# Optimization experiments

Measured on AMD Instinct MI355X. Metric: run time of the kernel, lower is better.

Reference implementation:

```python
import jax, jax.numpy as jnp
import numpy as np

ENC_DIM = 1024
NUM_HEADS = 16
HEAD_DIM = ENC_DIM // NUM_HEADS
D_FF = 4 * ENC_DIM
EPS = 1e-5


def _layernorm(x, g, b):
    mu = jnp.mean(x, axis=-1, keepdims=True)
    var = jnp.mean((x - mu) ** 2, axis=-1, keepdims=True)
    return (x - mu) * jax.lax.rsqrt(var + EPS) * g + b


def setup_inputs() -> dict:
    key = jax.random.key(0)
    ks = jax.random.split(key, 12)
    s = 1.0 / np.sqrt(ENC_DIM)
    sf = 1.0 / np.sqrt(D_FF)
    x = jax.random.normal(ks[0], (2, 2048, ENC_DIM), dtype=jnp.float32)
    return {
        "x": x,
        "ln1_g": jnp.ones((ENC_DIM,), jnp.float32),
        "ln1_b": jnp.zeros((ENC_DIM,), jnp.float32),
        "wq": jax.random.uniform(ks[1], (ENC_DIM, ENC_DIM), jnp.float32, -s, s),
        "bq": jax.random.uniform(ks[2], (ENC_DIM,), jnp.float32, -s, s),
        "wk": jax.random.uniform(ks[3], (ENC_DIM, ENC_DIM), jnp.float32, -s, s),
        "bk": jax.random.uniform(ks[4], (ENC_DIM,), jnp.float32, -s, s),
        "wv": jax.random.uniform(ks[5], (ENC_DIM, ENC_DIM), jnp.float32, -s, s),
        "bv": jax.random.uniform(ks[6], (ENC_DIM,), jnp.float32, -s, s),
        "wo": jax.random.uniform(ks[7], (ENC_DIM, ENC_DIM), jnp.float32, -s, s),
        "bo": jax.random.uniform(ks[8], (ENC_DIM,), jnp.float32, -s, s),
        "w1": jax.random.uniform(ks[9], (ENC_DIM, D_FF), jnp.float32, -s, s),
        "b1": jax.random.uniform(ks[10], (D_FF,), jnp.float32, -s, s),
        "w2": jax.random.uniform(ks[11], (D_FF, ENC_DIM), jnp.float32, -sf, sf),
        "b2": jnp.zeros((ENC_DIM,), jnp.float32),
        "ln2_g": jnp.ones((ENC_DIM,), jnp.float32),
        "ln2_b": jnp.zeros((ENC_DIM,), jnp.float32),
    }


def reference(x, ln1_g, ln1_b, wq, bq, wk, bk, wv, bv, wo, bo, w1, b1, w2, b2, ln2_g, ln2_b):
    B, S, D = x.shape
    h = _layernorm(x, ln1_g, ln1_b)
    # QKV projections -> (B, H, S, hd)
    def split_heads(t):
        return t.reshape(B, S, NUM_HEADS, HEAD_DIM).transpose(0, 2, 1, 3)
    q = split_heads(h @ wq + bq)
    k = split_heads(h @ wk + bk)
    v = split_heads(h @ wv + bv)
    scores = jnp.einsum("bhqd,bhkd->bhqk", q, k) / np.sqrt(HEAD_DIM)
    probs = jax.nn.softmax(scores, axis=-1)
    attn = jnp.einsum("bhqk,bhkd->bhqd", probs, v)
    attn = attn.transpose(0, 2, 1, 3).reshape(B, S, D)
    x = attn @ wo + bo + x  # residual 1
    h2 = _layernorm(x, ln2_g, ln2_b)
    mlp = jax.nn.gelu(h2 @ w1 + b1, approximate=False) @ w2 + b2
    return x + mlp
```

## Files before the change

### kernel.cpp

```cpp
#include <hip/hip_runtime.h>

typedef unsigned short u16;
typedef unsigned int u32;
typedef __bf16 bf16x8 __attribute__((ext_vector_type(8)));
typedef float floatx4 __attribute__((ext_vector_type(4)));

__device__ __forceinline__ u16 f2bf(float f) {
    u32 u = __float_as_uint(f);
    u = (u + 0x7FFFu + ((u >> 16) & 1u)) >> 16;
    return (u16)u;
}

__device__ __forceinline__ void gld_lds16(const u16* g, u16* l) {
    __builtin_amdgcn_global_load_lds(
        (const __attribute__((address_space(1))) u32*)g,
        (__attribute__((address_space(3))) u32*)l, 16, 0, 0);
}

__device__ __forceinline__ float gelu_exact(float v) {
    const float z = fabsf(v) * 0.70710678118f;
    const float t = __builtin_amdgcn_rcpf(1.0f + 0.3275911f * z);
    const float e = __builtin_amdgcn_exp2f(-z * z * 1.44269504f);
    float poly = 1.061405429f;
    poly = poly * t - 1.453152027f;
    poly = poly * t + 1.421413741f;
    poly = poly * t - 0.284496736f;
    poly = poly * t + 0.254829592f;
    float erfz = 1.0f - poly * t * e;
    erfz = copysignf(erfz, v);
    return 0.5f * v * (1.0f + erfz);
}

__global__ __launch_bounds__(256) void transpose_cvt4(
    const float* __restrict__ s0, const float* __restrict__ s1,
    const float* __restrict__ s2, const float* __restrict__ s3,
    u16* __restrict__ d0, u16* __restrict__ d1,
    u16* __restrict__ d2, u16* __restrict__ d3)
{
    __shared__ float t[32][33];
    const int z = blockIdx.z;
    const float* src = z == 0 ? s0 : (z == 1 ? s1 : (z == 2 ? s2 : s3));
    u16* dst = z == 0 ? d0 : (z == 1 ? d1 : (z == 2 ? d2 : d3));
    const int bm = blockIdx.x * 32, bk = blockIdx.y * 32;
    const int tx = threadIdx.x & 31, ty = threadIdx.x >> 5;
    #pragma unroll
    for (int i = ty; i < 32; i += 8)
        t[i][tx] = src[(long)(bk + i) * 1024 + bm + tx];
    __syncthreads();
    #pragma unroll
    for (int i = ty; i < 32; i += 8)
        dst[(long)(bm + i) * 1024 + bk + tx] = f2bf(t[tx][i]);
}

__global__ __launch_bounds__(256) void transpose_cvt(
    const float* __restrict__ src, u16* __restrict__ dst, int K, int M)
{
    __shared__ float t[32][33];
    const int bm = blockIdx.x * 32, bk = blockIdx.y * 32;
    const int tx = threadIdx.x & 31, ty = threadIdx.x >> 5;
    #pragma unroll
    for (int i = ty; i < 32; i += 8)
        t[i][tx] = src[(long)(bk + i) * M + bm + tx];
    __syncthreads();
    #pragma unroll
    for (int i = ty; i < 32; i += 8)
        dst[(long)(bm + i) * K + bk + tx] = f2bf(t[tx][i]);
}

__global__ __launch_bounds__(256) void ln_kernel(
    const float* __restrict__ x, const float* __restrict__ g,
    const float* __restrict__ bta, u16* __restrict__ out)
{
    const int row = blockIdx.x;
    const int tid = threadIdx.x;
    const float4 v = ((const float4*)(x + (long)row * 1024))[tid];
    float s  = v.x + v.y + v.z + v.w;
    float s2 = v.x*v.x + v.y*v.y + v.z*v.z + v.w*v.w;
    #pragma unroll
    for (int off = 1; off < 64; off <<= 1) {
        s  += __shfl_xor(s, off);
        s2 += __shfl_xor(s2, off);
    }
    __shared__ float red[8];
    const int wave = tid >> 6, lane = tid & 63;
    if (lane == 0) { red[wave] = s; red[4 + wave] = s2; }
    __syncthreads();
    s  = red[0] + red[1] + red[2] + red[3];
    s2 = red[4] + red[5] + red[6] + red[7];
    const float mu   = s * (1.0f / 1024.0f);
    const float var  = s2 * (1.0f / 1024.0f) - mu * mu;
    const float rstd = rsqrtf(var + 1e-5f);
    const int c = tid << 2;
    ushort4 o;
    o.x = f2bf((v.x - mu) * rstd * g[c + 0] + bta[c + 0]);
    o.y = f2bf((v.y - mu) * rstd * g[c + 1] + bta[c + 1]);
    o.z = f2bf((v.z - mu) * rstd * g[c + 2] + bta[c + 2]);
    o.w = f2bf((v.w - mu) * rstd * g[c + 3] + bta[c + 3]);
    ((ushort4*)(out + (long)row * 1024))[tid] = o;
}

__global__ __launch_bounds__(256) void add_kernel(
    float* __restrict__ out, const float* __restrict__ p1)
{
    const int t = blockIdx.x * 256 + threadIdx.x;
    const float4 a = ((const float4*)out)[t];
    const float4 c = ((const float4*)p1)[t];
    float4 o;
    o.x = a.x + c.x;
    o.y = a.y + c.y;
    o.z = a.z + c.z;
    o.w = a.w + c.w;
    ((float4*)out)[t] = o;
}

__global__ __launch_bounds__(256) void vtrans_kernel(
    const u16* __restrict__ V, u16* __restrict__ Vt)
{
    __shared__ u16 t[64][72];
    const int bh = blockIdx.y, s0 = blockIdx.x << 6;
    const int tid = threadIdx.x;
    const long base = (long)bh * 2048 * 64;
    const int row = tid >> 2, seg = tid & 3;
    *(uint4*)&t[row][seg << 3] =
        *(const uint4*)(V + base + (long)(s0 + row) * 64 + (seg << 3));
    *(uint4*)&t[row][(seg + 4) << 3] =
        *(const uint4*)(V + base + (long)(s0 + row) * 64 + ((seg + 4) << 3));
    __syncthreads();
    #pragma unroll
    for (int half = 0; half < 2; ++half) {
        const int sl = (seg + (half << 2)) << 3;
        u16 tmp[8];
        #pragma unroll
        for (int j = 0; j < 8; ++j) tmp[j] = t[sl + j][row];
        *(uint4*)(Vt + base + (long)row * 2048 + s0 + sl) = *(uint4*)tmp;
    }
}

template<int MODE, int BN>
__global__ __launch_bounds__(256) void gemm_kernel(
    const u16* __restrict__ A, const u16* __restrict__ Bt,
    const float* __restrict__ bias0, const float* __restrict__ bias1,
    const float* __restrict__ bias2, const float* __restrict__ res,
    float* __restrict__ part1, void* __restrict__ outv, int K, int M)
{
    constexpr int MS  = (BN == 128) ? 4 : 2;
    constexpr int NIB = (BN == 128) ? 4 : 2;
    __shared__ u16 As[128 * 64];
    __shared__ u16 Bs[BN * 64];
    const int tid = threadIdx.x, lane = tid & 63, wave = tid >> 6;
    const int wm = (BN == 128) ? ((wave >> 1) << 6) : (wave << 5);
    const int wn = (BN == 128) ? ((wave & 1) << 6) : 0;
    const int lrow = lane & 15, quad = lane >> 4;
    const int sl = lrow & 7;
    const long rowbase = (long)blockIdx.y * 128;
    const long colbase = (long)blockIdx.x * BN;
    int kstart = 0, kend = K;
    if constexpr (MODE == 3) {
        kstart = blockIdx.z * (K >> 1);
        kend   = kstart + (K >> 1);
    }

    const u16* gA[4]; int lA[4];
    #pragma unroll
    for (int i = 0; i < 4; ++i) {
        const int cid = (i << 6) + lane;
        const int rl = cid >> 3, p = cid & 7, q = p ^ (rl & 7);
        gA[i] = A + (rowbase + (wave << 5) + rl) * (long)K + kstart + (q << 3);
        lA[i] = ((wave << 5) + rl) * 64 + (p << 3);
    }
    const u16* gB[NIB]; int lB[NIB];
    #pragma unroll
    for (int i = 0; i < NIB; ++i) {
        const int cid = (i << 6) + lane;
        const int rl = cid >> 3, p = cid & 7, q = p ^ (rl & 7);
        const int rw = (BN == 128) ? (wave << 5) : (wave << 4);
        gB[i] = Bt + (colbase + rw + rl) * (long)K + kstart + (q << 3);
        lB[i] = (rw + rl) * 64 + (p << 3);
    }

    floatx4 acc[MS][4];
    #pragma unroll
    for (int i = 0; i < MS; ++i)
        #pragma unroll
        for (int j = 0; j < 4; ++j)
            acc[i][j] = floatx4{0.f, 0.f, 0.f, 0.f};

    for (int k0 = kstart; k0 < kend; k0 += 64) {
        __syncthreads();
        #pragma unroll
        for (int i = 0; i < 4; ++i) { gld_lds16(gA[i], As + lA[i]); gA[i] += 64; }
        #pragma unroll
        for (int i = 0; i < NIB; ++i) { gld_lds16(gB[i], Bs + lB[i]); gB[i] += 64; }
        __syncthreads();
        #pragma unroll
        for (int kc = 0; kc < 2; ++kc) {
            const int ph = (((kc << 2) + quad) ^ sl) << 3;
            bf16x8 af[MS], bf[4];
            #pragma unroll
            for (int ms = 0; ms < MS; ++ms)
                af[ms] = *(const bf16x8*)&As[(wm + (ms << 4) + lrow) * 64 + ph];
            #pragma unroll
            for (int ns = 0; ns < 4; ++ns)
                bf[ns] = *(const bf16x8*)&Bs[(wn + (ns << 4) + lrow) * 64 + ph];
            #pragma unroll
            for (int ms = 0; ms < MS; ++ms)
                #pragma unroll
                for (int ns = 0; ns < 4; ++ns)
                    acc[ms][ns] = __builtin_amdgcn_mfma_f32_16x16x32_bf16(
                        af[ms], bf[ns], acc[ms][ns], 0, 0, 0);
        }
    }

    float* tgt = nullptr;
    if constexpr (MODE == 3) tgt = blockIdx.z ? part1 : (float*)outv;
    #pragma unroll
    for (int ms = 0; ms < MS; ++ms) {
        #pragma unroll
        for (int ns = 0; ns < 4; ++ns) {
            const long col = colbase + wn + (ns << 4) + lrow;
            float bv = 0.f;
            if constexpr (MODE == 0) {
                const int which = (int)(col >> 10);
                const float* bp = which == 0 ? bias0 : (which == 1 ? bias1 : bias2);
                bv = bp[col & 1023];
            } else if constexpr (MODE == 1 || MODE == 2) {
                bv = bias0[col];
            }
            #pragma unroll
            for (int r = 0; r < 4; ++r) {
                const long row = rowbase + wm + (ms << 4) + (quad << 2) + r;
                float v = acc[ms][ns][r] + bv;
                if constexpr (MODE == 0) {
                    const long which = col >> 10;
                    if (which == 0) v *= 0.18033688f;
                    const long b = row >> 11, s = row & 2047;
                    const long h = (col >> 6) & 15, d = col & 63;
                    ((u16*)outv)[which * 4194304 + (((b << 4) + h) * 2048 + s) * 64 + d] = f2bf(v);
                } else if constexpr (MODE == 1) {
                    const long idx = row * M + col;
                    ((float*)outv)[idx] = v + res[idx];
                } else if constexpr (MODE == 2) {
                    ((u16*)outv)[row * M + col] = f2bf(gelu_exact(v));
                } else {
                    const long idx = row * M + col;
                    if (blockIdx.z == 0)
                        tgt[idx] = v + bias0[col] + res[idx];
                    else
                        tgt[idx] = v;
                }
            }
        }
    }
}

__global__ __launch_bounds__(256) void attn_kernel(
    const u16* __restrict__ Q, const u16* __restrict__ Kp,
    const u16* __restrict__ Vt, u16* __restrict__ O)
{
    __shared__ u16 Ks[2][4096];
    __shared__ u16 Vs[2][4096];
    __shared__ u16 Ps[4][2][16][72];
    const int tid = threadIdx.x, lane = tid & 63, wave = tid >> 6;
    const int lrow = lane & 15, quad = lane >> 4;
    const int bh = blockIdx.y;
    const long kvbase = (long)bh * 2048 * 64;
    const int qbase = (blockIdx.x << 7) + (wave << 5);

    const int srow = lane >> 3;
    const int schunk = (lane & 7) ^ srow;
    const int i0 = wave << 1;
    const u16* kg0 = Kp + kvbase + (long)(((i0 << 3) + srow) * 64 + (schunk << 3));
    const u16* kg1 = kg0 + 8 * 64;
    const u16* vg0 = Vt + kvbase + (long)(((i0 << 3) + srow) * 2048 + (schunk << 3));
    const u16* vg1 = vg0 + 8 * 2048;
    const int lofs = i0 << 9;

    bf16x8 qf[2][2];
    #pragma unroll
    for (int g = 0; g < 2; ++g)
        #pragma unroll
        for (int h = 0; h < 2; ++h)
            qf[g][h] = *(const bf16x8*)(Q + kvbase +
                (long)(qbase + (g << 4) + lrow) * 64 + (quad << 3) + (h << 5));

    int aoff[4][2];
    #pragma unroll
    for (int ns = 0; ns < 4; ++ns)
        #pragma unroll
        for (int h = 0; h < 2; ++h)
            aoff[ns][h] = ((ns << 4) + lrow) * 64 +
                          (((quad + (h << 2)) ^ (lrow & 7)) << 3);

    floatx4 oacc[2][4];
    #pragma unroll
    for (int g = 0; g < 2; ++g)
        #pragma unroll
        for (int ns = 0; ns < 4; ++ns)
            oacc[g][ns] = floatx4{0.f, 0.f, 0.f, 0.f};
    float lr[2] = {0.f, 0.f};

    gld_lds16(kg0, &Ks[0][lofs]);
    gld_lds16(kg1, &Ks[0][lofs + 512]);
    gld_lds16(vg0, &Vs[0][lofs]);
    gld_lds16(vg1, &Vs[0][lofs + 512]);
    kg0 += 4096; kg1 += 4096;
    int vofs = 64;

    for (int it = 0; it < 32; ++it) {
        const int cur = it & 1;
        __syncthreads();
        if (it < 31) {
            const int nxt = cur ^ 1;
            gld_lds16(kg0, &Ks[nxt][lofs]);
            gld_lds16(kg1, &Ks[nxt][lofs + 512]);
            gld_lds16(vg0 + vofs, &Vs[nxt][lofs]);
            gld_lds16(vg1 + vofs, &Vs[nxt][lofs + 512]);
            kg0 += 4096; kg1 += 4096; vofs += 64;
        }
        const u16* ks = &Ks[cur][0];
        const u16* vs = &Vs[cur][0];

        floatx4 st[2][4];
        __builtin_amdgcn_s_setprio(1);
        #pragma unroll
        for (int ns = 0; ns < 4; ++ns) {
            const bf16x8 af0 = *(const bf16x8*)&ks[aoff[ns][0]];
            const bf16x8 af1 = *(const bf16x8*)&ks[aoff[ns][1]];
            floatx4 z = floatx4{0.f, 0.f, 0.f, 0.f};
            st[0][ns] = __builtin_amdgcn_mfma_f32_16x16x32_bf16(af0, qf[0][0], z, 0, 0, 0);
            st[0][ns] = __builtin_amdgcn_mfma_f32_16x16x32_bf16(af1, qf[0][1], st[0][ns], 0, 0, 0);
            st[1][ns] = __builtin_amdgcn_mfma_f32_16x16x32_bf16(af0, qf[1][0], z, 0, 0, 0);
            st[1][ns] = __builtin_amdgcn_mfma_f32_16x16x32_bf16(af1, qf[1][1], st[1][ns], 0, 0, 0);
        }
        __builtin_amdgcn_s_setprio(0);

        bf16x8 pf[2][2];
        #pragma unroll
        for (int g = 0; g < 2; ++g) {
            float rs = 0.f;
            #pragma unroll
            for (int ns = 0; ns < 4; ++ns) {
                const float p0 = __builtin_amdgcn_exp2f(st[g][ns][0]);
                const float p1 = __builtin_amdgcn_exp2f(st[g][ns][1]);
                const float p2 = __builtin_amdgcn_exp2f(st[g][ns][2]);
                const float p3 = __builtin_amdgcn_exp2f(st[g][ns][3]);
                rs += (p0 + p1) + (p2 + p3);
                uint2 w;
                w.x = __builtin_amdgcn_perm(__float_as_uint(p1) + 0x8000u,
                                            __float_as_uint(p0) + 0x8000u, 0x07060302u);
                w.y = __builtin_amdgcn_perm(__float_as_uint(p3) + 0x8000u,
                                            __float_as_uint(p2) + 0x8000u, 0x07060302u);
                *(uint2*)&Ps[wave][g][lrow][(ns << 4) + (quad << 2)] = w;
            }
            rs += __shfl_xor(rs, 16);
            rs += __shfl_xor(rs, 32);
            lr[g] += rs;
            pf[g][0] = *(const bf16x8*)&Ps[wave][g][lrow][quad << 3];
            pf[g][1] = *(const bf16x8*)&Ps[wave][g][lrow][(quad << 3) + 32];
        }

        __builtin_amdgcn_s_setprio(1);
        #pragma unroll
        for (int ns = 0; ns < 4; ++ns) {
            const bf16x8 vf0 = *(const bf16x8*)&vs[aoff[ns][0]];
            const bf16x8 vf1 = *(const bf16x8*)&vs[aoff[ns][1]];
            #pragma unroll
            for (int g = 0; g < 2; ++g) {
                oacc[g][ns] = __builtin_amdgcn_mfma_f32_16x16x32_bf16(
                    pf[g][0], vf0, oacc[g][ns], 0, 0, 0);
                oacc[g][ns] = __builtin_amdgcn_mfma_f32_16x16x32_bf16(
                    pf[g][1], vf1, oacc[g][ns], 0, 0, 0);
            }
        }
        __builtin_amdgcn_s_setprio(0);
    }

    const int b = bh >> 4, h = bh & 15;
    #pragma unroll
    for (int g = 0; g < 2; ++g) {
        float linv[4];
        #pragma unroll
        for (int r = 0; r < 4; ++r)
            linv[r] = 1.0f / __shfl(lr[g], (quad << 2) + r);
        #pragma unroll
        for (int ns = 0; ns < 4; ++ns)
            #pragma unroll
            for (int r = 0; r < 4; ++r) {
                const int q = qbase + (g << 4) + (quad << 2) + r;
                const long token = (long)b * 2048 + q;
                O[token * 1024 + (h << 6) + (ns << 4) + lrow] =
                    f2bf(oacc[g][ns][r] * linv[r]);
            }
    }
}

extern "C" void kernel_launch(void* const* d_in, const int* in_sizes, int n_in,
                              void* d_out, int out_size, void* d_ws, size_t ws_size,
                              hipStream_t stream)
{
    const float* x     = (const float*)d_in[0];
    const float* ln1_g = (const float*)d_in[1];
    const float* ln1_b = (const float*)d_in[2];
    const float* wq    = (const float*)d_in[3];
    const float* bq    = (const float*)d_in[4];
    const float* wk    = (const float*)d_in[5];
    const float* bk    = (const float*)d_in[6];
    const float* wv    = (const float*)d_in[7];
    const float* bv    = (const float*)d_in[8];
    const float* wo    = (const float*)d_in[9];
    const float* bo    = (const float*)d_in[10];
    const float* w1    = (const float*)d_in[11];
    const float* b1    = (const float*)d_in[12];
    const float* w2    = (const float*)d_in[13];
    const float* b2    = (const float*)d_in[14];
    const float* ln2_g = (const float*)d_in[15];
    const float* ln2_b = (const float*)d_in[16];
    float* out = (float*)d_out;

    char* w = (char*)d_ws;
    const size_t MB = 1024 * 1024;
    u16*   wqkvt = (u16*)(w + 0);
    u16*   wot   = (u16*)(w + 6  * MB);
    u16*   w1t   = (u16*)(w + 8  * MB);
    u16*   w2t   = (u16*)(w + 16 * MB);
    u16*   h1    = (u16*)(w + 24 * MB);
    u16*   qkvb  = (u16*)(w + 32 * MB);
    u16*   vtb   = (u16*)(w + 56 * MB);
    float* x1    = (float*)(w + 64 * MB);
    float* part1 = (float*)(w + 80 * MB);
    u16*   ffb   = (u16*)(w + 32 * MB);
    u16*   qb = qkvb;
    u16*   kb = qkvb + 4194304;
    u16*   vb = qkvb + 8388608;

    transpose_cvt4<<<dim3(32, 32, 4), 256, 0, stream>>>(
        wq, wk, wv, wo, wqkvt, wqkvt + 1048576, wqkvt + 2097152, wot);
    transpose_cvt<<<dim3(128, 32), 256, 0, stream>>>(w1, w1t, 1024, 4096);
    transpose_cvt<<<dim3(32, 128), 256, 0, stream>>>(w2, w2t, 4096, 1024);

    ln_kernel<<<4096, 256, 0, stream>>>(x, ln1_g, ln1_b, h1);

    gemm_kernel<0, 128><<<dim3(24, 32), 256, 0, stream>>>(
        h1, wqkvt, bq, bk, bv, nullptr, nullptr, qkvb, 1024, 3072);

    vtrans_kernel<<<dim3(32, 32), 256, 0, stream>>>(vb, vtb);

    attn_kernel<<<dim3(16, 32), 256, 0, stream>>>(qb, kb, vtb, h1);

    gemm_kernel<1, 64><<<dim3(16, 32), 256, 0, stream>>>(
        h1, wot, bo, nullptr, nullptr, x, nullptr, x1, 1024, 1024);

    ln_kernel<<<4096, 256, 0, stream>>>(x1, ln2_g, ln2_b, h1);

    gemm_kernel<2, 128><<<dim3(32, 32), 256, 0, stream>>>(
        h1, w1t, b1, nullptr, nullptr, nullptr, nullptr, ffb, 1024, 4096);

    gemm_kernel<3, 64><<<dim3(16, 32, 2), 256, 0, stream>>>(
        ffb, w2t, b2, nullptr, nullptr, x1, part1, out, 4096, 1024);

    add_kernel<<<4096, 256, 0, stream>>>(out, part1);
}
```

Baseline: 386.6 us.

## Use 512-thread attention blocks with one 16-row query group per wave and swizzled block order

The attention kernel moves from 4 waves each handling 32 query rows to 8 waves each handling 16 rows. K/V tile loading is split so half the waves load K and half load V. The launch becomes a 1-D grid with remapped block indices, likely to spread heads across XCDs or improve L2 locality. This doubles wave-level parallelism per block and lowers per-wave registers, but each wave now reuses every K/V fragment it reads from LDS for only one query group instead of two.

```diff
diff --git a/kernel.cpp b/kernel.cpp
--- a/kernel.cpp
+++ b/kernel.cpp
@@ -253,35 +253,41 @@
     }
 }
 
-__global__ __launch_bounds__(256) void attn_kernel(
+__global__ __launch_bounds__(512) void attn_kernel(
     const u16* __restrict__ Q, const u16* __restrict__ Kp,
     const u16* __restrict__ Vt, u16* __restrict__ O)
 {
     __shared__ u16 Ks[2][4096];
     __shared__ u16 Vs[2][4096];
-    __shared__ u16 Ps[4][2][16][72];
+    __shared__ u16 Ps[8][16][72];
     const int tid = threadIdx.x, lane = tid & 63, wave = tid >> 6;
     const int lrow = lane & 15, quad = lane >> 4;
-    const int bh = blockIdx.y;
+
+    const int lin = blockIdx.x;
+    const int nl  = ((lin & 7) << 6) + (lin >> 3);
+    const int bh  = nl >> 4;
+    const int qt  = nl & 15;
     const long kvbase = (long)bh * 2048 * 64;
-    const int qbase = (blockIdx.x << 7) + (wave << 5);
+    const int qbase = (qt << 7) + (wave << 4);
 
     const int srow = lane >> 3;
     const int schunk = (lane & 7) ^ srow;
-    const int i0 = wave << 1;
-    const u16* kg0 = Kp + kvbase + (long)(((i0 << 3) + srow) * 64 + (schunk << 3));
-    const u16* kg1 = kg0 + 8 * 64;
-    const u16* vg0 = Vt + kvbase + (long)(((i0 << 3) + srow) * 2048 + (schunk << 3));
-    const u16* vg1 = vg0 + 8 * 2048;
-    const int lofs = i0 << 9;
-
-    bf16x8 qf[2][2];
-    #pragma unroll
-    for (int g = 0; g < 2; ++g)
-        #pragma unroll
-        for (int h = 0; h < 2; ++h)
-            qf[g][h] = *(const bf16x8*)(Q + kvbase +
-                (long)(qbase + (g << 4) + lrow) * 64 + (quad << 3) + (h << 5));
+    const int c = wave & 3;
+    const bool isV = wave >= 4;
+    const int lofs = c << 10;
+    const u16* g0 = isV
+        ? (Vt + kvbase + (long)(((c << 4) + srow) * 2048 + (schunk << 3)))
+        : (Kp + kvbase + (long)(((c << 4) + srow) * 64   + (schunk << 3)));
+    const u16* g1 = g0 + (isV ? 8 * 2048 : 8 * 64);
+    const int gstep = isV ? 64 : 4096;
+    u16* lb0 = isV ? &Vs[0][lofs] : &Ks[0][lofs];
+    u16* lb1 = isV ? &Vs[1][lofs] : &Ks[1][lofs];
+
+    bf16x8 qf[2];
+    #pragma unroll
+    for (int h = 0; h < 2; ++h)
+        qf[h] = *(const bf16x8*)(Q + kvbase +
+            (long)(qbase + lrow) * 64 + (quad << 3) + (h << 5));
 
     int aoff[4][2];
     #pragma unroll
@@ -291,107 +297,86 @@
             aoff[ns][h] = ((ns << 4) + lrow) * 64 +
                           (((quad + (h << 2)) ^ (lrow & 7)) << 3);
 
-    floatx4 oacc[2][4];
-    #pragma unroll
-    for (int g = 0; g < 2; ++g)
-        #pragma unroll
-        for (int ns = 0; ns < 4; ++ns)
-            oacc[g][ns] = floatx4{0.f, 0.f, 0.f, 0.f};
-    float lr[2] = {0.f, 0.f};
-
-    gld_lds16(kg0, &Ks[0][lofs]);
-    gld_lds16(kg1, &Ks[0][lofs + 512]);
-    gld_lds16(vg0, &Vs[0][lofs]);
-    gld_lds16(vg1, &Vs[0][lofs + 512]);
-    kg0 += 4096; kg1 += 4096;
-    int vofs = 64;
+    floatx4 oacc[4];
+    #pragma unroll
+    for (int ns = 0; ns < 4; ++ns)
+        oacc[ns] = floatx4{0.f, 0.f, 0.f, 0.f};
+    float lr = 0.f;
+
+    gld_lds16(g0, lb0);
+    gld_lds16(g1, lb0 + 512);
+    g0 += gstep; g1 += gstep;
 
     for (int it = 0; it < 32; ++it) {
         const int cur = it & 1;
         __syncthreads();
         if (it < 31) {
-            const int nxt = cur ^ 1;
-            gld_lds16(kg0, &Ks[nxt][lofs]);
-            gld_lds16(kg1, &Ks[nxt][lofs + 512]);
-            gld_lds16(vg0 + vofs, &Vs[nxt][lofs]);
-            gld_lds16(vg1 + vofs, &Vs[nxt][lofs + 512]);
-            kg0 += 4096; kg1 += 4096; vofs += 64;
+            u16* dst = cur ? lb0 : lb1;
+            gld_lds16(g0, dst);
+            gld_lds16(g1, dst + 512);
+            g0 += gstep; g1 += gstep;
         }
         const u16* ks = &Ks[cur][0];
         const u16* vs = &Vs[cur][0];
 
-        floatx4 st[2][4];
+        floatx4 st[4];
         __builtin_amdgcn_s_setprio(1);
         #pragma unroll
         for (int ns = 0; ns < 4; ++ns) {
             const bf16x8 af0 = *(const bf16x8*)&ks[aoff[ns][0]];
             const bf16x8 af1 = *(const bf16x8*)&ks[aoff[ns][1]];
             floatx4 z = floatx4{0.f, 0.f, 0.f, 0.f};
-            st[0][ns] = __builtin_amdgcn_mfma_f32_16x16x32_bf16(af0, qf[0][0], z, 0, 0, 0);
-            st[0][ns] = __builtin_amdgcn_mfma_f32_16x16x32_bf16(af1, qf[0][1], st[0][ns], 0, 0, 0);
-            st[1][ns] = __builtin_amdgcn_mfma_f32_16x16x32_bf16(af0, qf[1][0], z, 0, 0, 0);
-            st[1][ns] = __builtin_amdgcn_mfma_f32_16x16x32_bf16(af1, qf[1][1], st[1][ns], 0, 0, 0);
+            st[ns] = __builtin_amdgcn_mfma_f32_16x16x32_bf16(af0, qf[0], z, 0, 0, 0);
+            st[ns] = __builtin_amdgcn_mfma_f32_16x16x32_bf16(af1, qf[1], st[ns], 0, 0, 0);
         }
         __builtin_amdgcn_s_setprio(0);
 
-        bf16x8 pf[2][2];
-        #pragma unroll
-        for (int g = 0; g < 2; ++g) {
-            float rs = 0.f;
-            #pragma unroll
-            for (int ns = 0; ns < 4; ++ns) {
-                const float p0 = __builtin_amdgcn_exp2f(st[g][ns][0]);
-                const float p1 = __builtin_amdgcn_exp2f(st[g][ns][1]);
-                const float p2 = __builtin_amdgcn_exp2f(st[g][ns][2]);
-                const float p3 = __builtin_amdgcn_exp2f(st[g][ns][3]);
-                rs += (p0 + p1) + (p2 + p3);
-                uint2 w;
-                w.x = __builtin_amdgcn_perm(__float_as_uint(p1) + 0x8000u,
-                                            __float_as_uint(p0) + 0x8000u, 0x07060302u);
-                w.y = __builtin_amdgcn_perm(__float_as_uint(p3) + 0x8000u,
-                                            __float_as_uint(p2) + 0x8000u, 0x07060302u);
-                *(uint2*)&Ps[wave][g][lrow][(ns << 4) + (quad << 2)] = w;
-            }
-            rs += __shfl_xor(rs, 16);
-            rs += __shfl_xor(rs, 32);
-            lr[g] += rs;
-            pf[g][0] = *(const bf16x8*)&Ps[wave][g][lrow][quad << 3];
-            pf[g][1] = *(const bf16x8*)&Ps[wave][g][lrow][(quad << 3) + 32];
-        }
+        float rs = 0.f;
+        #pragma unroll
+        for (int ns = 0; ns < 4; ++ns) {
+            const float p0 = __builtin_amdgcn_exp2f(st[ns][0]);
+            const float p1 = __builtin_amdgcn_exp2f(st[ns][1]);
+            const float p2 = __builtin_amdgcn_exp2f(st[ns][2]);
+            const float p3 = __builtin_amdgcn_exp2f(st[ns][3]);
+            rs += (p0 + p1) + (p2 + p3);
+            uint2 w;
+            w.x = __builtin_amdgcn_perm(__float_as_uint(p1) + 0x8000u,
+                                        __float_as_uint(p0) + 0x8000u, 0x07060302u);
+            w.y = __builtin_amdgcn_perm(__float_as_uint(p3) + 0x8000u,
+                                        __float_as_uint(p2) + 0x8000u, 0x07060302u);
+            *(uint2*)&Ps[wave][lrow][(ns << 4) + (quad << 2)] = w;
+        }
+        rs += __shfl_xor(rs, 16);
+        rs += __shfl_xor(rs, 32);
+        lr += rs;
+        const bf16x8 pf0 = *(const bf16x8*)&Ps[wave][lrow][quad << 3];
+        const bf16x8 pf1 = *(const bf16x8*)&Ps[wave][lrow][(quad << 3) + 32];
 
         __builtin_amdgcn_s_setprio(1);
         #pragma unroll
         for (int ns = 0; ns < 4; ++ns) {
             const bf16x8 vf0 = *(const bf16x8*)&vs[aoff[ns][0]];
             const bf16x8 vf1 = *(const bf16x8*)&vs[aoff[ns][1]];
-            #pragma unroll
-            for (int g = 0; g < 2; ++g) {
-                oacc[g][ns] = __builtin_amdgcn_mfma_f32_16x16x32_bf16(
-                    pf[g][0], vf0, oacc[g][ns], 0, 0, 0);
-                oacc[g][ns] = __builtin_amdgcn_mfma_f32_16x16x32_bf16(
-                    pf[g][1], vf1, oacc[g][ns], 0, 0, 0);
-            }
+            oacc[ns] = __builtin_amdgcn_mfma_f32_16x16x32_bf16(pf0, vf0, oacc[ns], 0, 0, 0);
+            oacc[ns] = __builtin_amdgcn_mfma_f32_16x16x32_bf16(pf1, vf1, oacc[ns], 0, 0, 0);
         }
         __builtin_amdgcn_s_setprio(0);
     }
 
     const int b = bh >> 4, h = bh & 15;
-    #pragma unroll
-    for (int g = 0; g < 2; ++g) {
-        float linv[4];
-        #pragma unroll
-        for (int r = 0; r < 4; ++r)
-            linv[r] = 1.0f / __shfl(lr[g], (quad << 2) + r);
-        #pragma unroll
-        for (int ns = 0; ns < 4; ++ns)
-            #pragma unroll
-            for (int r = 0; r < 4; ++r) {
-                const int q = qbase + (g << 4) + (quad << 2) + r;
-                const long token = (long)b * 2048 + q;
-                O[token * 1024 + (h << 6) + (ns << 4) + lrow] =
-                    f2bf(oacc[g][ns][r] * linv[r]);
-            }
-    }
+    float linv[4];
+    #pragma unroll
+    for (int r = 0; r < 4; ++r)
+        linv[r] = 1.0f / __shfl(lr, (quad << 2) + r);
+    #pragma unroll
+    for (int ns = 0; ns < 4; ++ns)
+        #pragma unroll
+        for (int r = 0; r < 4; ++r) {
+            const int q = qbase + (quad << 2) + r;
+            const long token = (long)b * 2048 + q;
+            O[token * 1024 + (h << 6) + (ns << 4) + lrow] =
+                f2bf(oacc[ns][r] * linv[r]);
+        }
 }
 
 extern "C" void kernel_launch(void* const* d_in, const int* in_sizes, int n_in,
@@ -445,7 +430,7 @@
 
     vtrans_kernel<<<dim3(32, 32), 256, 0, stream>>>(vb, vtb);
 
-    attn_kernel<<<dim3(16, 32), 256, 0, stream>>>(qb, kb, vtb, h1);
+    attn_kernel<<<dim3(512), 512, 0, stream>>>(qb, kb, vtb, h1);
 
     gemm_kernel<1, 64><<<dim3(16, 32), 256, 0, stream>>>(
         h1, wot, bo, nullptr, nullptr, x, nullptr, x1, 1024, 1024);
```

Result: no change. 383.0 us (-0.9%).
